# Kernel optimization log

Hardware: AMD Instinct MI355X
Metric: run time of the kernel (lower is better)

Reference implementation:

```python
import jax, jax.numpy as jnp
import numpy as np

B, N, C, H, HD, HH, WW, K, ALPHA = 8, 4096, 256, 8, 32, 64, 64, 5, 4.0


def setup_inputs() -> dict:
    key = jax.random.key(0)
    ks = jax.random.split(key, 6)
    return {
        "x": jax.random.normal(ks[0], (B, N, C), jnp.float32),
        "W_qg": jax.random.normal(ks[1], (C, 2 * C), jnp.float32) * 0.02,
        "W_kv": jax.random.normal(ks[2], (C, 2 * C), jnp.float32) * 0.02,
        "W_proj": jax.random.normal(ks[3], (C, C), jnp.float32) * 0.02,
        "b_proj": jnp.zeros((C,), jnp.float32),
        "dwc_w": jax.random.normal(ks[4], (HD, 1, K, K), jnp.float32) * 0.05,
        "dwc_b": jnp.zeros((HD,), jnp.float32),
        "power_p": jnp.zeros((1, H, 1, HD), jnp.float32),
    }


def _safe_pow(x, p):
    # x >= 0 (post-relu). 0**p == 0 for p > 0; guard base so grads stay finite.
    xs = jnp.where(x > 0, x, 1.0)
    return jnp.where(x > 0, xs ** p, 0.0)


def reference(x, W_qg, W_kv, W_proj, b_proj, dwc_w, dwc_b, power_p):
    qg = x @ W_qg                                  # (B,N,2C)
    q, g = qg[..., :C], qg[..., C:]
    kv = x @ W_kv                                  # (B,N,2C)
    k = kv[..., :C].reshape(B, N, H, HD).transpose(0, 2, 1, 3)   # (B,H,N,hd)
    v = kv[..., C:].reshape(B, N, H, HD).transpose(0, 2, 1, 3)
    q = q.reshape(B, N, H, HD).transpose(0, 2, 1, 3)

    power = 1.0 + ALPHA * jax.nn.sigmoid(power_p)  # (1,H,1,hd)
    # x_s = q_pos@kv_s + q_neg@kv_s = (q_pos+q_neg)@kv_s, kv_s = (k_pos+k_neg)^T v_s
    q_sum = _safe_pow(jax.nn.relu(q), power) + _safe_pow(jax.nn.relu(-q), power)
    k_sum = _safe_pow(jax.nn.relu(k), power) + _safe_pow(jax.nn.relu(-k), power)

    v_s, v_o = v[..., : HD // 2], v[..., HD // 2 :]
    kv_s = jnp.einsum('bhnd,bhne->bhde', k_sum, v_s)
    kv_o = jnp.einsum('bhnd,bhne->bhde', k_sum, v_o)
    x_s = jnp.einsum('bhnd,bhde->bhne', q_sum, kv_s)
    x_o = jnp.einsum('bhnd,bhde->bhne', q_sum, kv_o)
    x_att = jnp.concatenate([x_s, x_o], -1).transpose(0, 2, 1, 3).reshape(B, N, C)

    # depthwise conv branch: exact layout replication of torch permute/reshape chain
    v_img = v.transpose(0, 2, 1, 3).reshape(B * H, HD, HH, WW)
    pad = K // 2
    v_loc = jax.lax.conv_general_dilated(
        v_img, dwc_w, (1, 1), [(pad, pad), (pad, pad)],
        feature_group_count=HD,
        dimension_numbers=('NCHW', 'OIHW', 'NCHW')) + dwc_b[None, :, None, None]
    v_loc = v_loc.reshape(B, H, HD, N).transpose(0, 2, 1, 3).reshape(B, C, N).transpose(0, 2, 1)

    return ((x_att + v_loc) * g) @ W_proj + b_proj
```

## Files before the change

### kernel.cpp

```cpp
#include <hip/hip_runtime.h>
#include <hip/hip_bf16.h>
#include <math.h>

#define B_ 8
#define N_ 4096
#define C_ 256
#define H_ 8
#define HD_ 32
#define BN_ (B_ * N_)
#define E_ ((size_t)BN_ * C_)

typedef __attribute__((ext_vector_type(8))) short short8;
typedef __attribute__((ext_vector_type(4))) float f32x4;

__device__ __forceinline__ float b2f(__hip_bfloat16 x) { return __bfloat162float(x); }

__device__ __forceinline__ void gl_lds16(const void* gp, void* lp) {
    __builtin_amdgcn_global_load_lds(
        (const __attribute__((address_space(1))) unsigned int*)gp,
        (__attribute__((address_space(3))) unsigned int*)lp,
        16, 0, 0);
}

__device__ __forceinline__ float fast_abspow(float v, float p) {
    float av = fabsf(v);
    return (av > 0.f) ? __builtin_amdgcn_exp2f(p * __builtin_amdgcn_logf(av)) : 0.f;
}

__device__ __forceinline__ float bf_lo(unsigned u) { return __uint_as_float(u << 16); }
__device__ __forceinline__ float bf_hi(unsigned u) { return __uint_as_float(u & 0xffff0000u); }
__device__ __forceinline__ unsigned short f2bfbits(float f) {
    __hip_bfloat16 h = __float2bfloat16(f);
    return *(unsigned short*)&h;
}
__device__ __forceinline__ unsigned pack2(float lo, float hi) {
    return (unsigned)f2bfbits(lo) | ((unsigned)f2bfbits(hi) << 16);
}

__global__ __launch_bounds__(256) void cvt_all(
    const float* __restrict__ x, const float* __restrict__ Wqg,
    const float* __restrict__ Wkv, const float* __restrict__ Wp,
    const float* __restrict__ pp,
    __hip_bfloat16* __restrict__ xb, __hip_bfloat16* __restrict__ Wt1,
    __hip_bfloat16* __restrict__ Wt2, float* __restrict__ powers,
    float* __restrict__ kv_mat2)
{
    int t = threadIdx.x;
    int bid0 = blockIdx.x;
    if (bid0 < 4096) {
        size_t i = ((size_t)bid0 * 256 + t) * 8;
        float4 a = *(const float4*)&x[i];
        float4 b = *(const float4*)&x[i + 4];
        uint4 o = {pack2(a.x, a.y), pack2(a.z, a.w), pack2(b.x, b.y), pack2(b.z, b.w)};
        *(uint4*)&xb[i] = o;
        return;
    }
    int bid = bid0 - 4096;
    if (bid == 80) {
        powers[t] = 1.0f + 4.0f / (1.0f + expf(-pp[t]));
        return;
    }
    if (bid >= 81) {
        ((float4*)kv_mat2)[(size_t)(bid - 81) * 256 + t] = (float4){0.f, 0.f, 0.f, 0.f};
        return;
    }
    __shared__ float tile[64][65];
    const float* src;
    __hip_bfloat16* dst;
    int scols, tr, tc, dn0;
    if (bid < 32)      { src = Wqg; scols = 512; tr = bid >> 3;        tc = bid & 7;        dst = Wt1; dn0 = tc * 64; }
    else if (bid < 64) { src = Wkv; scols = 512; tr = (bid - 32) >> 3; tc = (bid - 32) & 7; dst = Wt1; dn0 = 512 + tc * 64; }
    else               { src = Wp;  scols = 256; tr = (bid - 64) >> 2; tc = (bid - 64) & 3; dst = Wt2; dn0 = tc * 64; }
    int tx = t & 63, ty = t >> 6;
    #pragma unroll
    for (int i = 0; i < 16; i++) {
        int r = ty + i * 4;
        tile[r][tx] = src[(size_t)(tr * 64 + r) * scols + tc * 64 + tx];
    }
    __syncthreads();
    #pragma unroll
    for (int i = 0; i < 16; i++) {
        int n_local = ty + i * 4;
        dst[(size_t)(dn0 + n_local) * 256 + tr * 64 + tx] = __float2bfloat16(tile[tx][n_local]);
    }
}

__global__ __launch_bounds__(256) void gemm1_mfma(
    const __hip_bfloat16* __restrict__ xb, const __hip_bfloat16* __restrict__ Wt1,
    const float* __restrict__ powers,
    __hip_bfloat16* __restrict__ q16, __hip_bfloat16* __restrict__ k16,
    __hip_bfloat16* __restrict__ g16, __hip_bfloat16* __restrict__ v16)
{
    __shared__ __align__(16) unsigned short As[128 * 64];
    __shared__ __align__(16) unsigned short Bs[128 * 64];
    int t = threadIdx.x;
    int w = t >> 6, l = t & 63;
    int bswz = (blockIdx.x & 7) * 256 + (blockIdx.x >> 3);
    int row0 = (bswz >> 3) * 128;
    int colb = bswz & 7;
    int col0 = colb * 128;
    int wm = (w >> 1) * 64, wn = (w & 1) * 64;
    int lane15 = l & 15, quad = l >> 4;
    int sr8 = l >> 3;
    int sc = ((l & 7) ^ sr8) * 8;
    int r7 = lane15 & 7;

    f32x4 acc[4][4];
    #pragma unroll
    for (int mi = 0; mi < 4; mi++)
        #pragma unroll
        for (int ni = 0; ni < 4; ni++) acc[mi][ni] = (f32x4){0.f, 0.f, 0.f, 0.f};

    for (int k0 = 0; k0 < 256; k0 += 64) {
        #pragma unroll
        for (int j = 0; j < 4; j++) {
            int rowl = j * 32 + w * 8 + sr8;
            gl_lds16(&xb[(size_t)(row0 + rowl) * 256 + k0 + sc],
                     &As[(j * 32 + w * 8) * 64]);
            gl_lds16(&Wt1[(size_t)(col0 + rowl) * 256 + k0 + sc],
                     &Bs[(j * 32 + w * 8) * 64]);
        }
        __syncthreads();
        #pragma unroll
        for (int kh = 0; kh < 2; kh++) {
            int cs_k = ((kh * 4 + quad) ^ r7) * 8;
            short8 a[4], b[4];
            #pragma unroll
            for (int mi = 0; mi < 4; mi++)
                a[mi] = *(const short8*)&As[(wm + mi * 16 + lane15) * 64 + cs_k];
            #pragma unroll
            for (int ni = 0; ni < 4; ni++)
                b[ni] = *(const short8*)&Bs[(wn + ni * 16 + lane15) * 64 + cs_k];
            #pragma unroll
            for (int mi = 0; mi < 4; mi++)
                #pragma unroll
                for (int ni = 0; ni < 4; ni++)
                    acc[mi][ni] = __builtin_amdgcn_mfma_f32_16x16x32_bf16(a[mi], b[ni], acc[mi][ni], 0, 0, 0);
        }
        __syncthreads();
    }

    int region = colb >> 1;
    bool dopow = (region == 0) || (region == 2);
    __hip_bfloat16* dst = (region == 0) ? q16 : (region == 1) ? g16 : (region == 2) ? k16 : v16;
    #pragma unroll
    for (int mi = 0; mi < 4; mi++) {
        #pragma unroll
        for (int ni = 0; ni < 4; ni++) {
            int row = row0 + wm + mi * 16 + quad * 4;
            int col = col0 + wn + ni * 16 + lane15;
            int c255 = col & 255;
            float p = powers[c255];
            #pragma unroll
            for (int r = 0; r < 4; r++) {
                float v = acc[mi][ni][r];
                float o = dopow ? fast_abspow(v, p) : v;
                dst[(size_t)(row + r) * 256 + c255] = __float2bfloat16(o);
            }
        }
    }
}

__global__ __launch_bounds__(256) void kvmat_mfma(
    const __hip_bfloat16* __restrict__ k16, const __hip_bfloat16* __restrict__ v16,
    float* __restrict__ kv_mat2)
{
    __shared__ __align__(16) unsigned short KV[2][32][136];
    int t = threadIdx.x;
    int w = t >> 6, l = t & 63;
    int lane15 = l & 15, quad = l >> 4;
    int bid = blockIdx.x;
    int pair = bid >> 3, seg = bid & 7;
    int b = pair >> 3, h = pair & 7;
    int nloc = t & 127, cs = (t >> 7) * 16;

    f32x4 acc[2][2];
    #pragma unroll
    for (int di = 0; di < 2; di++)
        #pragma unroll
        for (int ei = 0; ei < 2; ei++) acc[di][ei] = (f32x4){0.f, 0.f, 0.f, 0.f};

    const size_t base = (size_t)b * N_ * 256 + h * 32 + cs;
    for (int c4 = 0; c4 < 4; c4++) {
        int n0 = seg * 512 + c4 * 128;
        const uint4* kp = (const uint4*)(k16 + base + (size_t)(n0 + nloc) * 256);
        uint4 ka = kp[0], kb = kp[1];
        const uint4* vp = (const uint4*)(v16 + base + (size_t)(n0 + nloc) * 256);
        uint4 va = vp[0], vb = vp[1];
        __syncthreads();
        unsigned kw[8] = {ka.x, ka.y, ka.z, ka.w, kb.x, kb.y, kb.z, kb.w};
        unsigned vw[8] = {va.x, va.y, va.z, va.w, vb.x, vb.y, vb.z, vb.w};
        #pragma unroll
        for (int j = 0; j < 8; j++) {
            KV[0][cs + 2 * j][nloc]     = (unsigned short)(kw[j] & 0xffffu);
            KV[0][cs + 2 * j + 1][nloc] = (unsigned short)(kw[j] >> 16);
            KV[1][cs + 2 * j][nloc]     = (unsigned short)(vw[j] & 0xffffu);
            KV[1][cs + 2 * j + 1][nloc] = (unsigned short)(vw[j] >> 16);
        }
        __syncthreads();
        int nb = w * 32 + quad * 8;
        short8 a[2], bb[2];
        #pragma unroll
        for (int di = 0; di < 2; di++)
            a[di] = *(const short8*)&KV[0][di * 16 + lane15][nb];
        #pragma unroll
        for (int ei = 0; ei < 2; ei++)
            bb[ei] = *(const short8*)&KV[1][ei * 16 + lane15][nb];
        #pragma unroll
        for (int di = 0; di < 2; di++)
            #pragma unroll
            for (int ei = 0; ei < 2; ei++)
                acc[di][ei] = __builtin_amdgcn_mfma_f32_16x16x32_bf16(a[di], bb[ei], acc[di][ei], 0, 0, 0);
    }

    __syncthreads();
    float* red = (float*)KV;
    #pragma unroll
    for (int di = 0; di < 2; di++)
        #pragma unroll
        for (int ei = 0; ei < 2; ei++) {
            int e = ei * 16 + lane15;
            #pragma unroll
            for (int r = 0; r < 4; r++) {
                int d = di * 16 + quad * 4 + r;
                red[w * 1056 + e * 33 + d] = acc[di][ei][r];
            }
        }
    __syncthreads();
    #pragma unroll
    for (int j = 0; j < 4; j++) {
        int o = j * 256 + t;
        int e = o >> 5, d = o & 31;
        float s = red[e * 33 + d] + red[1056 + e * 33 + d]
                + red[2112 + e * 33 + d] + red[3168 + e * 33 + d];
        atomicAdd(&kv_mat2[(size_t)b * 8192 + e * 256 + h * 32 + d], s);
    }
}

__global__ __launch_bounds__(256) void conv_kernel(
    const __hip_bfloat16* __restrict__ v16,
    const float* __restrict__ w, const float* __restrict__ bias,
    __hip_bfloat16* __restrict__ vloc)
{
    __shared__ __align__(16) float img[64 * 72];
    __shared__ float wl[25];
    int t = threadIdx.x;
    int gid = blockIdx.x;
    int DD = gid & 31;
    if (t < 128) {
        int row = t >> 1, side = (t & 1) * 68;
        *(float4*)&img[row * 72 + side] = (float4){0.f, 0.f, 0.f, 0.f};
    }
    if (t < 25) wl[t] = w[DD * 25 + t];
    {
        int row = t >> 2, colb = (t & 3) * 16;
        const uint4* src = (const uint4*)(v16 + (size_t)gid * 4096 + row * 64 + colb);
        uint4 u0 = src[0], u1 = src[1];
        float4* d = (float4*)&img[row * 72 + 4 + colb];
        d[0] = (float4){bf_lo(u0.x), bf_hi(u0.x), bf_lo(u0.y), bf_hi(u0.y)};
        d[1] = (float4){bf_lo(u0.z), bf_hi(u0.z), bf_lo(u0.w), bf_hi(u0.w)};
        d[2] = (float4){bf_lo(u1.x), bf_hi(u1.x), bf_lo(u1.y), bf_hi(u1.y)};
        d[3] = (float4){bf_lo(u1.z), bf_hi(u1.z), bf_lo(u1.w), bf_hi(u1.w)};
    }
    __syncthreads();
    float bs = bias[DD];
    int x0 = (t & 15) * 4, yb = t >> 4;
    #pragma unroll
    for (int s = 0; s < 4; s++) {
        int y = yb + s * 16;
        float a0 = bs, a1 = bs, a2 = bs, a3 = bs;
        #pragma unroll
        for (int ky = 0; ky < 5; ky++) {
            int row = y + ky - 2;
            if (row < 0 || row >= 64) continue;
            const float* rp = &img[row * 72 + x0];
            float4 w0 = *(const float4*)rp;
            float4 w1 = *(const float4*)(rp + 4);
            float4 w2 = *(const float4*)(rp + 8);
            float win[12] = {w0.x, w0.y, w0.z, w0.w, w1.x, w1.y, w1.z, w1.w,
                             w2.x, w2.y, w2.z, w2.w};
            #pragma unroll
            for (int kx = 0; kx < 5; kx++) {
                float wt = wl[ky * 5 + kx];
                a0 += wt * win[2 + kx];
                a1 += wt * win[3 + kx];
                a2 += wt * win[4 + kx];
                a3 += wt * win[5 + kx];
            }
        }
        unsigned lo = pack2(a0, a1);
        unsigned hi = pack2(a2, a3);
        *(uint2*)(vloc + (size_t)gid * 4096 + y * 64 + x0) = (uint2){lo, hi};
    }
}

#define A2P 264
__global__ __launch_bounds__(256) void att_gemm2(
    const __hip_bfloat16* __restrict__ q16, const float* __restrict__ kv_mat2,
    const __hip_bfloat16* __restrict__ vloc, const __hip_bfloat16* __restrict__ g16,
    const __hip_bfloat16* __restrict__ Wt2, const float* __restrict__ bp,
    float* __restrict__ out)
{
    __shared__ __align__(16) unsigned short QA[64 * A2P];
    __shared__ __align__(16) unsigned short Bs[256 * 64];
    int t = threadIdx.x;
    int w = t >> 6, l = t & 63;
    int r0 = blockIdx.x * 64;
    int b = r0 >> 12, n0 = r0 & 4095;
    int lane15 = l & 15, quad = l >> 4;
    int h0 = w * 2;
    int sr8 = l >> 3;
    int sc = ((l & 7) ^ sr8) * 8;
    int r7 = lane15 & 7;

    {
        const uint4* qsrc = (const uint4*)(q16 + (size_t)(r0 + (t >> 2)) * 256 + (t & 3) * 64);
        uint4* qdst = (uint4*)&QA[(t >> 2) * A2P + (t & 3) * 64];
        #pragma unroll
        for (int j = 0; j < 8; j++) qdst[j] = qsrc[j];
    }
    __syncthreads();

    short8 afr[4][2];
    #pragma unroll
    for (int m = 0; m < 4; m++)
        #pragma unroll
        for (int hh = 0; hh < 2; hh++)
            afr[m][hh] = *(const short8*)&QA[(m * 16 + lane15) * A2P + (h0 + hh) * 32 + quad * 8];

    short8 bfr[2][2];
    #pragma unroll
    for (int hh = 0; hh < 2; hh++) {
        #pragma unroll
        for (int nt = 0; nt < 2; nt++) {
            const float4* kp = (const float4*)(kv_mat2 + (size_t)b * 8192 +
                (size_t)(nt * 16 + lane15) * 256 + (h0 + hh) * 32 + quad * 8);
            float4 ka = kp[0], kb = kp[1];
            short8 bb;
            bb[0] = (short)f2bfbits(ka.x); bb[1] = (short)f2bfbits(ka.y);
            bb[2] = (short)f2bfbits(ka.z); bb[3] = (short)f2bfbits(ka.w);
            bb[4] = (short)f2bfbits(kb.x); bb[5] = (short)f2bfbits(kb.y);
            bb[6] = (short)f2bfbits(kb.z); bb[7] = (short)f2bfbits(kb.w);
            bfr[hh][nt] = bb;
        }
    }

    f32x4 ac[4][2][2];
    #pragma unroll
    for (int m = 0; m < 4; m++)
        #pragma unroll
        for (int hh = 0; hh < 2; hh++)
            #pragma unroll
            for (int nt = 0; nt < 2; nt++)
                ac[m][hh][nt] = __builtin_amdgcn_mfma_f32_16x16x32_bf16(
                    afr[m][hh], bfr[hh][nt], (f32x4){0.f, 0.f, 0.f, 0.f}, 0, 0, 0);

    #pragma unroll
    for (int m = 0; m < 4; m++) {
        #pragma unroll
        for (int hh = 0; hh < 2; hh++) {
            #pragma unroll
            for (int nt = 0; nt < 2; nt++) {
                int col = (h0 + hh) * 32 + nt * 16 + lane15;
                int rowb = m * 16 + quad * 4;
                size_t img = ((size_t)((b * 8 + (col & 7)) * 32 + (col >> 3))) * 4096 + n0 + rowb;
                uint2 vv = *(const uint2*)(vloc + img);
                float vl[4] = {bf_lo(vv.x), bf_hi(vv.x), bf_lo(vv.y), bf_hi(vv.y)};
                #pragma unroll
                for (int i = 0; i < 4; i++) {
                    float gg = b2f(g16[(size_t)(r0 + rowb + i) * 256 + col]);
                    float val = (ac[m][hh][nt][i] + vl[i]) * gg;
                    QA[(rowb + i) * A2P + col] = f2bfbits(val);
                }
            }
        }
    }

    int wm = (w & 1) * 32, wn = (w >> 1) * 128;
    f32x4 acc2[2][8];
    #pragma unroll
    for (int mi = 0; mi < 2; mi++)
        #pragma unroll
        for (int ni = 0; ni < 8; ni++) acc2[mi][ni] = (f32x4){0.f, 0.f, 0.f, 0.f};

    for (int k0 = 0; k0 < 256; k0 += 64) {
        __syncthreads();
        #pragma unroll
        for (int j = 0; j < 8; j++) {
            int rowl = j * 32 + w * 8 + sr8;
            gl_lds16(&Wt2[(size_t)rowl * 256 + k0 + sc],
                     &Bs[(j * 32 + w * 8) * 64]);
        }
        __syncthreads();
        #pragma unroll
        for (int h2 = 0; h2 < 2; h2++) {
            int cs_k = ((h2 * 4 + quad) ^ r7) * 8;
            short8 a[2], bb[8];
            #pragma unroll
            for (int mi = 0; mi < 2; mi++)
                a[mi] = *(const short8*)&QA[(wm + mi * 16 + lane15) * A2P + k0 + h2 * 32 + quad * 8];
            #pragma unroll
            for (int ni = 0; ni < 8; ni++)
                bb[ni] = *(const short8*)&Bs[(wn + ni * 16 + lane15) * 64 + cs_k];
            #pragma unroll
            for (int mi = 0; mi < 2; mi++)
                #pragma unroll
                for (int ni = 0; ni < 8; ni++)
                    acc2[mi][ni] = __builtin_amdgcn_mfma_f32_16x16x32_bf16(a[mi], bb[ni], acc2[mi][ni], 0, 0, 0);
        }
    }

    #pragma unroll
    for (int mi = 0; mi < 2; mi++) {
        #pragma unroll
        for (int ni = 0; ni < 8; ni++) {
            int row = r0 + wm + mi * 16 + quad * 4;
            int col = wn + ni * 16 + lane15;
            float bv = bp[col];
            #pragma unroll
            for (int r = 0; r < 4; r++)
                out[(size_t)(row + r) * 256 + col] = acc2[mi][ni][r] + bv;
        }
    }
}

extern "C" void kernel_launch(void* const* d_in, const int* in_sizes, int n_in,
                              void* d_out, int out_size, void* d_ws, size_t ws_size,
                              hipStream_t stream) {
    const float* x      = (const float*)d_in[0];
    const float* W_qg   = (const float*)d_in[1];
    const float* W_kv   = (const float*)d_in[2];
    const float* W_proj = (const float*)d_in[3];
    const float* b_proj = (const float*)d_in[4];
    const float* dwc_w  = (const float*)d_in[5];
    const float* dwc_b  = (const float*)d_in[6];
    const float* pow_p  = (const float*)d_in[7];
    float* out = (float*)d_out;

    float* ws = (float*)d_ws;
    const size_t E = E_;
    __hip_bfloat16* q16  = (__hip_bfloat16*)ws;
    __hip_bfloat16* k16  = (__hip_bfloat16*)(ws + E / 2);
    __hip_bfloat16* g16  = (__hip_bfloat16*)(ws + E);
    __hip_bfloat16* v16  = (__hip_bfloat16*)(ws + 3 * E / 2);
    __hip_bfloat16* xb   = (__hip_bfloat16*)(ws + 2 * E);
    __hip_bfloat16* vl16 = (__hip_bfloat16*)(ws + 5 * E / 2);
    float* kv_mat2 = ws + 3 * E;
    __hip_bfloat16* Wt1 = (__hip_bfloat16*)(kv_mat2 + 65536);
    __hip_bfloat16* Wt2 = Wt1 + 262144;
    float* powers = (float*)(Wt2 + 65536);

    cvt_all<<<4096 + 81 + 64, 256, 0, stream>>>(x, W_qg, W_kv, W_proj, pow_p, xb, Wt1, Wt2, powers, kv_mat2);
    gemm1_mfma<<<2048, 256, 0, stream>>>(xb, Wt1, powers, q16, k16, g16, v16);
    kvmat_mfma<<<512, 256, 0, stream>>>(k16, v16, kv_mat2);
    conv_kernel<<<2048, 256, 0, stream>>>(v16, dwc_w, dwc_b, vl16);
    att_gemm2<<<512, 256, 0, stream>>>(q16, kv_mat2, vl16, g16, Wt2, b_proj, out);
}
```

Before: 176.4 us.

## Stage gemm1 epilogue through LDS for vector stores; merge kvmat and conv launches

The gemm1 epilogue now writes the bf16 outputs into a swizzled LDS tile that reuses the A/B staging buffer, then emits 16-byte coalesced global stores instead of scattered 2-byte stores. The kv-matrix reduction and the depthwise conv kernels are combined into one launch that branches on block index and shares a raw LDS buffer. This removes one kernel launch and the gap between the two, and lets both workloads fill the GPU together. The cost is an extra LDS round trip and barrier in the gemm1 epilogue, and the merged kernel now holds the larger of the two LDS footprints, which may lower occupancy for the conv blocks.

```diff
diff --git a/kernel.cpp b/kernel.cpp
--- a/kernel.cpp
+++ b/kernel.cpp
@@ -91,8 +91,9 @@
     __hip_bfloat16* __restrict__ q16, __hip_bfloat16* __restrict__ k16,
     __hip_bfloat16* __restrict__ g16, __hip_bfloat16* __restrict__ v16)
 {
-    __shared__ __align__(16) unsigned short As[128 * 64];
-    __shared__ __align__(16) unsigned short Bs[128 * 64];
+    __shared__ __align__(16) unsigned short ABs[128 * 128];
+    unsigned short* As = ABs;
+    unsigned short* Bs = ABs + 128 * 64;
     int t = threadIdx.x;
     int w = t >> 6, l = t & 63;
     int bswz = (blockIdx.x & 7) * 256 + (blockIdx.x >> 3);
@@ -143,109 +144,119 @@
     int region = colb >> 1;
     bool dopow = (region == 0) || (region == 2);
     __hip_bfloat16* dst = (region == 0) ? q16 : (region == 1) ? g16 : (region == 2) ? k16 : v16;
+    int cbase = col0 & 255;
     #pragma unroll
     for (int mi = 0; mi < 4; mi++) {
         #pragma unroll
         for (int ni = 0; ni < 4; ni++) {
-            int row = row0 + wm + mi * 16 + quad * 4;
-            int col = col0 + wn + ni * 16 + lane15;
-            int c255 = col & 255;
-            float p = powers[c255];
+            int rowb = wm + mi * 16 + quad * 4;
+            int coll = wn + ni * 16 + lane15;
+            float p = powers[cbase + coll];
+            int cchunk = coll >> 3, cin = coll & 7;
             #pragma unroll
             for (int r = 0; r < 4; r++) {
+                int rl = rowb + r;
                 float v = acc[mi][ni][r];
                 float o = dopow ? fast_abspow(v, p) : v;
-                dst[(size_t)(row + r) * 256 + c255] = __float2bfloat16(o);
+                ABs[rl * 128 + ((cchunk ^ (rl & 15)) << 3) + cin] = f2bfbits(o);
             }
         }
     }
-}
-
-__global__ __launch_bounds__(256) void kvmat_mfma(
+    __syncthreads();
+    #pragma unroll
+    for (int j = 0; j < 8; j++) {
+        int g = j * 256 + t;
+        int rl = g >> 4, chunk = g & 15;
+        uint4 vv = *(const uint4*)&ABs[rl * 128 + ((chunk ^ (rl & 15)) << 3)];
+        *(uint4*)&dst[(size_t)(row0 + rl) * 256 + cbase + chunk * 8] = vv;
+    }
+}
+
+__global__ __launch_bounds__(256) void kvconv_kernel(
     const __hip_bfloat16* __restrict__ k16, const __hip_bfloat16* __restrict__ v16,
-    float* __restrict__ kv_mat2)
-{
-    __shared__ __align__(16) unsigned short KV[2][32][136];
-    int t = threadIdx.x;
-    int w = t >> 6, l = t & 63;
-    int lane15 = l & 15, quad = l >> 4;
-    int bid = blockIdx.x;
-    int pair = bid >> 3, seg = bid & 7;
-    int b = pair >> 3, h = pair & 7;
-    int nloc = t & 127, cs = (t >> 7) * 16;
-
-    f32x4 acc[2][2];
-    #pragma unroll
-    for (int di = 0; di < 2; di++)
-        #pragma unroll
-        for (int ei = 0; ei < 2; ei++) acc[di][ei] = (f32x4){0.f, 0.f, 0.f, 0.f};
-
-    const size_t base = (size_t)b * N_ * 256 + h * 32 + cs;
-    for (int c4 = 0; c4 < 4; c4++) {
-        int n0 = seg * 512 + c4 * 128;
-        const uint4* kp = (const uint4*)(k16 + base + (size_t)(n0 + nloc) * 256);
-        uint4 ka = kp[0], kb = kp[1];
-        const uint4* vp = (const uint4*)(v16 + base + (size_t)(n0 + nloc) * 256);
-        uint4 va = vp[0], vb = vp[1];
-        __syncthreads();
-        unsigned kw[8] = {ka.x, ka.y, ka.z, ka.w, kb.x, kb.y, kb.z, kb.w};
-        unsigned vw[8] = {va.x, va.y, va.z, va.w, vb.x, vb.y, vb.z, vb.w};
-        #pragma unroll
-        for (int j = 0; j < 8; j++) {
-            KV[0][cs + 2 * j][nloc]     = (unsigned short)(kw[j] & 0xffffu);
-            KV[0][cs + 2 * j + 1][nloc] = (unsigned short)(kw[j] >> 16);
-            KV[1][cs + 2 * j][nloc]     = (unsigned short)(vw[j] & 0xffffu);
-            KV[1][cs + 2 * j + 1][nloc] = (unsigned short)(vw[j] >> 16);
-        }
-        __syncthreads();
-        int nb = w * 32 + quad * 8;
-        short8 a[2], bb[2];
-        #pragma unroll
-        for (int di = 0; di < 2; di++)
-            a[di] = *(const short8*)&KV[0][di * 16 + lane15][nb];
-        #pragma unroll
-        for (int ei = 0; ei < 2; ei++)
-            bb[ei] = *(const short8*)&KV[1][ei * 16 + lane15][nb];
-        #pragma unroll
-        for (int di = 0; di < 2; di++)
-            #pragma unroll
-            for (int ei = 0; ei < 2; ei++)
-                acc[di][ei] = __builtin_amdgcn_mfma_f32_16x16x32_bf16(a[di], bb[ei], acc[di][ei], 0, 0, 0);
-    }
-
-    __syncthreads();
-    float* red = (float*)KV;
-    #pragma unroll
-    for (int di = 0; di < 2; di++)
-        #pragma unroll
-        for (int ei = 0; ei < 2; ei++) {
-            int e = ei * 16 + lane15;
-            #pragma unroll
-            for (int r = 0; r < 4; r++) {
-                int d = di * 16 + quad * 4 + r;
-                red[w * 1056 + e * 33 + d] = acc[di][ei][r];
-            }
-        }
-    __syncthreads();
-    #pragma unroll
-    for (int j = 0; j < 4; j++) {
-        int o = j * 256 + t;
-        int e = o >> 5, d = o & 31;
-        float s = red[e * 33 + d] + red[1056 + e * 33 + d]
-                + red[2112 + e * 33 + d] + red[3168 + e * 33 + d];
-        atomicAdd(&kv_mat2[(size_t)b * 8192 + e * 256 + h * 32 + d], s);
-    }
-}
-
-__global__ __launch_bounds__(256) void conv_kernel(
-    const __hip_bfloat16* __restrict__ v16,
+    float* __restrict__ kv_mat2,
     const float* __restrict__ w, const float* __restrict__ bias,
     __hip_bfloat16* __restrict__ vloc)
 {
-    __shared__ __align__(16) float img[64 * 72];
-    __shared__ float wl[25];
+    __shared__ __align__(16) unsigned char smraw[18560];
     int t = threadIdx.x;
-    int gid = blockIdx.x;
+
+    if (blockIdx.x < 512) {
+        unsigned short (*KV)[32][136] = (unsigned short (*)[32][136])smraw;
+        int w_ = t >> 6, l = t & 63;
+        int lane15 = l & 15, quad = l >> 4;
+        int bid = blockIdx.x;
+        int pair = bid >> 3, seg = bid & 7;
+        int b = pair >> 3, h = pair & 7;
+        int nloc = t & 127, cs = (t >> 7) * 16;
+
+        f32x4 acc[2][2];
+        #pragma unroll
+        for (int di = 0; di < 2; di++)
+            #pragma unroll
+            for (int ei = 0; ei < 2; ei++) acc[di][ei] = (f32x4){0.f, 0.f, 0.f, 0.f};
+
+        const size_t base = (size_t)b * N_ * 256 + h * 32 + cs;
+        for (int c4 = 0; c4 < 4; c4++) {
+            int n0 = seg * 512 + c4 * 128;
+            const uint4* kp = (const uint4*)(k16 + base + (size_t)(n0 + nloc) * 256);
+            uint4 ka = kp[0], kb = kp[1];
+            const uint4* vp = (const uint4*)(v16 + base + (size_t)(n0 + nloc) * 256);
+            uint4 va = vp[0], vb = vp[1];
+            __syncthreads();
+            unsigned kw[8] = {ka.x, ka.y, ka.z, ka.w, kb.x, kb.y, kb.z, kb.w};
+            unsigned vw[8] = {va.x, va.y, va.z, va.w, vb.x, vb.y, vb.z, vb.w};
+            #pragma unroll
+            for (int j = 0; j < 8; j++) {
+                KV[0][cs + 2 * j][nloc]     = (unsigned short)(kw[j] & 0xffffu);
+                KV[0][cs + 2 * j + 1][nloc] = (unsigned short)(kw[j] >> 16);
+                KV[1][cs + 2 * j][nloc]     = (unsigned short)(vw[j] & 0xffffu);
+                KV[1][cs + 2 * j + 1][nloc] = (unsigned short)(vw[j] >> 16);
+            }
+            __syncthreads();
+            int nb = w_ * 32 + quad * 8;
+            short8 a[2], bb[2];
+            #pragma unroll
+            for (int di = 0; di < 2; di++)
+                a[di] = *(const short8*)&KV[0][di * 16 + lane15][nb];
+            #pragma unroll
+            for (int ei = 0; ei < 2; ei++)
+                bb[ei] = *(const short8*)&KV[1][ei * 16 + lane15][nb];
+            #pragma unroll
+            for (int di = 0; di < 2; di++)
+                #pragma unroll
+                for (int ei = 0; ei < 2; ei++)
+                    acc[di][ei] = __builtin_amdgcn_mfma_f32_16x16x32_bf16(a[di], bb[ei], acc[di][ei], 0, 0, 0);
+        }
+
+        __syncthreads();
+        float* red = (float*)smraw;
+        #pragma unroll
+        for (int di = 0; di < 2; di++)
+            #pragma unroll
+            for (int ei = 0; ei < 2; ei++) {
+                int e = ei * 16 + lane15;
+                #pragma unroll
+                for (int r = 0; r < 4; r++) {
+                    int d = di * 16 + quad * 4 + r;
+                    red[w_ * 1056 + e * 33 + d] = acc[di][ei][r];
+                }
+            }
+        __syncthreads();
+        #pragma unroll
+        for (int j = 0; j < 4; j++) {
+            int o = j * 256 + t;
+            int e = o >> 5, d = o & 31;
+            float s = red[e * 33 + d] + red[1056 + e * 33 + d]
+                    + red[2112 + e * 33 + d] + red[3168 + e * 33 + d];
+            atomicAdd(&kv_mat2[(size_t)b * 8192 + e * 256 + h * 32 + d], s);
+        }
+        return;
+    }
+
+    float* img = (float*)smraw;
+    float* wl  = (float*)(smraw + 18432);
+    int gid = blockIdx.x - 512;
     int DD = gid & 31;
     if (t < 128) {
         int row = t >> 1, side = (t & 1) * 68;
@@ -452,7 +463,6 @@
 
     cvt_all<<<4096 + 81 + 64, 256, 0, stream>>>(x, W_qg, W_kv, W_proj, pow_p, xb, Wt1, Wt2, powers, kv_mat2);
     gemm1_mfma<<<2048, 256, 0, stream>>>(xb, Wt1, powers, q16, k16, g16, v16);
-    kvmat_mfma<<<512, 256, 0, stream>>>(k16, v16, kv_mat2);
-    conv_kernel<<<2048, 256, 0, stream>>>(v16, dwc_w, dwc_b, vl16);
+    kvconv_kernel<<<512 + 2048, 256, 0, stream>>>(k16, v16, kv_mat2, dwc_w, dwc_b, vl16);
     att_gemm2<<<512, 256, 0, stream>>>(q16, kv_mat2, vl16, g16, Wt2, b_proj, out);
 }
```

After: 171.1 us. 1.03x faster.
